# Performance work log

Hardware: AMD Instinct MI355X
Metric: run time of the kernel (lower is better)

The kernel has to match this reference:

```python
import jax, jax.numpy as jnp
import numpy as np

DIM = 1024
HEADS = 16
HEAD_DIM = DIM // HEADS
D_FF = 4 * DIM
EPS = 1e-5


def _layernorm(x, g, b):
    mu = jnp.mean(x, axis=-1, keepdims=True)
    var = jnp.mean(jnp.square(x - mu), axis=-1, keepdims=True)
    return (x - mu) * jax.lax.rsqrt(var + EPS) * g + b


def setup_inputs() -> dict:
    key = jax.random.key(0)
    ks = jax.random.split(key, 8)
    s = 0.02
    return {
        "x": jax.random.normal(ks[0], (2, 2048, DIM), dtype=jnp.float32),
        "Wqkv": jax.random.normal(ks[1], (DIM, 3 * DIM), dtype=jnp.float32) * s,
        "bqkv": jnp.zeros((3 * DIM,), dtype=jnp.float32),
        "Wout": jax.random.normal(ks[2], (DIM, DIM), dtype=jnp.float32) * s,
        "bout": jnp.zeros((DIM,), dtype=jnp.float32),
        "W1": jax.random.normal(ks[3], (DIM, D_FF), dtype=jnp.float32) * s,
        "b1": jnp.zeros((D_FF,), dtype=jnp.float32),
        "W2": jax.random.normal(ks[4], (D_FF, DIM), dtype=jnp.float32) * s,
        "b2": jnp.zeros((DIM,), dtype=jnp.float32),
        "g1": jnp.ones((DIM,), dtype=jnp.float32),
        "be1": jnp.zeros((DIM,), dtype=jnp.float32),
        "g2": jnp.ones((DIM,), dtype=jnp.float32),
        "be2": jnp.zeros((DIM,), dtype=jnp.float32),
    }


def reference(x, Wqkv, bqkv, Wout, bout, W1, b1, W2, b2, g1, be1, g2, be2):
    B, T, C = x.shape
    # --- multi-head self-attention (explicit QK^T softmax, no mask/cache) ---
    qkv = (x @ Wqkv + bqkv).reshape(B, T, 3, HEADS, HEAD_DIM)
    q = qkv[:, :, 0].transpose(0, 2, 1, 3)  # (B,H,T,hd)
    k = qkv[:, :, 1].transpose(0, 2, 1, 3)
    v = qkv[:, :, 2].transpose(0, 2, 1, 3)
    scale = HEAD_DIM ** -0.5
    scores = jnp.einsum("bhqd,bhkd->bhqk", q, k) * scale  # (B,H,T,T)
    attn = jax.nn.softmax(scores, axis=-1)
    o = jnp.einsum("bhqk,bhkd->bhqd", attn, v)
    o = o.transpose(0, 2, 1, 3).reshape(B, T, C)
    attn_out = o @ Wout + bout
    # --- Post-LN: LN applied to sublayer output, then residual ---
    x = x + _layernorm(attn_out, g1, be1)
    # --- FFN with exact GELU ---
    h = jax.nn.gelu(x @ W1 + b1, approximate=False)
    ffn_out = h @ W2 + b2
    x = x + _layernorm(ffn_out, g2, be2)
    return x
```

## Files before the change

### kernel.cpp

```cpp
#include <hip/hip_runtime.h>
#include <cstdint>
#include <cstddef>

#define DIM 1024
#define HEADS 16
#define HD 64
#define DFF 4096
#define TSEQ 2048
#define EPS 1e-5f

#define WAITCNT_VM4 0xF74
#define WAITCNT_VM0 0xF70
#define WAITCNT_VM8 0xF78
#define WAITCNT_VM4_LGKM0 0x074
#define WAITCNT_VM0_LGKM0 0x070
#define WAITCNT_LGKM0 0xC07F

typedef __bf16 bf16x8 __attribute__((ext_vector_type(8)));
typedef float floatx4 __attribute__((ext_vector_type(4)));

__device__ __forceinline__ unsigned short f2bf(float f) {
  union { float f; unsigned int u; } v; v.f = f;
  return (unsigned short)((v.u + 0x7FFFu + ((v.u >> 16) & 1u)) >> 16);
}

__device__ __forceinline__ float exp2_fast(float x) {
#if __has_builtin(__builtin_amdgcn_exp2f)
  return __builtin_amdgcn_exp2f(x);
#else
  float r;
  asm("v_exp_f32 %0, %1" : "=v"(r) : "v"(x));
  return r;
#endif
}

__device__ __forceinline__ float gelu_f(float v) {
  const float u = v * (0.7978845608f + 0.0356774081f * v * v);
  const float e = __expf(2.0f * u);
  const float t = 1.0f - 2.0f / (e + 1.0f);
  return 0.5f * v * (1.0f + t);
}

__device__ __forceinline__ void async16(const void* g, void* l) {
  __builtin_amdgcn_global_load_lds(
      (const __attribute__((address_space(1))) void*)g,
      (__attribute__((address_space(3))) void*)l, 16, 0, 0);
}

__global__ __launch_bounds__(256) void prep_all(const float* __restrict__ x,
                                                const float* __restrict__ Wqkv,
                                                const float* __restrict__ Wout,
                                                const float* __restrict__ W1,
                                                const float* __restrict__ W2,
                                                unsigned short* __restrict__ xb,
                                                unsigned short* __restrict__ WqkvT,
                                                unsigned short* __restrict__ WoutT,
                                                unsigned short* __restrict__ W1T,
                                                unsigned short* __restrict__ W2T) {
  const int bid = blockIdx.x;
  const int tid = threadIdx.x;
  if (bid < 4096) {
    const int i = bid * 256 + tid;
    float4 v = ((const float4*)x)[i];
    ushort4 o;
    o.x = f2bf(v.x); o.y = f2bf(v.y); o.z = f2bf(v.z); o.w = f2bf(v.w);
    ((ushort4*)xb)[i] = o;
    return;
  }
  int id = bid - 4096;
  const float* src; unsigned short* dst; int R, C, gx;
  if (id < 3072)      {            src = Wqkv; dst = WqkvT; R = 1024; C = 3072; gx = 96; }
  else if (id < 4096) { id -= 3072; src = Wout; dst = WoutT; R = 1024; C = 1024; gx = 32; }
  else if (id < 8192) { id -= 4096; src = W1;   dst = W1T;   R = 1024; C = 4096; gx = 128; }
  else                { id -= 8192; src = W2;   dst = W2T;   R = 4096; C = 1024; gx = 32; }
  const int c0 = (id % gx) * 32, r0 = (id / gx) * 32;
  const int tx = tid & 31, ty = tid >> 5;
  __shared__ float tile[32][33];
#pragma unroll
  for (int i = 0; i < 32; i += 8)
    tile[ty + i][tx] = src[(size_t)(r0 + ty + i) * C + c0 + tx];
  __syncthreads();
#pragma unroll
  for (int i = 0; i < 32; i += 8)
    dst[(size_t)(c0 + ty + i) * R + r0 + tx] = f2bf(tile[tx][ty + i]);
}

#define PIPELINED_KLOOP(NIT, STRIDE_EXPR)                                           \
  auto issue = [&](int s, int k0) {                                                  \
    async16(Ab0 + k0, &lds[s][tid * 8]);                                             \
    async16(Ab1 + k0, &lds[s][2048 + tid * 8]);                                      \
    async16(Bb0 + k0, &lds[s][4096 + tid * 8]);                                      \
    async16(Bb1 + k0, &lds[s][6144 + tid * 8]);                                      \
  };                                                                                 \
  issue(0, 0);                                                                       \
  issue(1, 32);                                                                      \
  int sidx = 0;                                                                      \
  for (int k = 0; k < (NIT); k++) {                                                  \
    if (k < (NIT)-1) __builtin_amdgcn_s_waitcnt(WAITCNT_VM4);                        \
    else             __builtin_amdgcn_s_waitcnt(WAITCNT_VM0);                        \
    __builtin_amdgcn_s_barrier();                                                    \
    if (k + 2 < (NIT)) {                                                             \
      int s2 = sidx + 2; if (s2 >= 3) s2 -= 3;                                       \
      issue(s2, (k + 2) * 32);                                                       \
    }                                                                                \
    bf16x8 af[4], bg[4];                                                             \
    _Pragma("unroll")                                                                \
    for (int mi = 0; mi < 4; mi++)                                                   \
      af[mi] = *(const bf16x8*)&lds[sidx][(wm + mi * 16 + l16) * 32 + quad * 8];     \
    _Pragma("unroll")                                                                \
    for (int ni = 0; ni < 4; ni++)                                                   \
      bg[ni] = *(const bf16x8*)&lds[sidx][4096 + (wn + ni * 16 + l16) * 32 + quad * 8]; \
    _Pragma("unroll")                                                                \
    for (int mi = 0; mi < 4; mi++)                                                   \
      _Pragma("unroll")                                                              \
      for (int ni = 0; ni < 4; ni++)                                                 \
        acc[mi][ni] =                                                                \
            __builtin_amdgcn_mfma_f32_16x16x32_bf16(af[mi], bg[ni], acc[mi][ni], 0, 0, 0); \
    sidx = (sidx == 2) ? 0 : sidx + 1;                                               \
  }

template <int EPI>
__global__ __launch_bounds__(256) void gemm_bt(const unsigned short* __restrict__ A,
                                               const unsigned short* __restrict__ Bt,
                                               const float* __restrict__ bias,
                                               void* __restrict__ Cout,
                                               int M, int N, int K) {
  __shared__ unsigned short lds[3][8192];
  const int tid = threadIdx.x;
  const int bm = blockIdx.y * 128, bn = blockIdx.x * 128;
  const int wave = tid >> 6, lane = tid & 63;
  const int l16 = lane & 15, quad = lane >> 4;
  const int wm = (wave >> 1) * 64, wn = (wave & 1) * 64;

  floatx4 acc[4][4] = {};

  const int srow = tid >> 2;
  const int scol = (tid & 3) * 8;

  const unsigned short* Ab0 = A + (size_t)(bm + srow) * K + scol;
  const unsigned short* Ab1 = A + (size_t)(bm + 64 + srow) * K + scol;
  const unsigned short* Bb0 = Bt + (size_t)(bn + srow) * K + scol;
  const unsigned short* Bb1 = Bt + (size_t)(bn + 64 + srow) * K + scol;

  const int nit = K >> 5;
  PIPELINED_KLOOP(nit, 32)
  __syncthreads();

  if (EPI == 0) {
#pragma unroll
    for (int ni = 0; ni < 4; ni++) {
      const int col = bn + wn + ni * 16 + l16;
      const float bv = bias[col];
#pragma unroll
      for (int mi = 0; mi < 4; mi++) {
        const int row0 = bm + wm + mi * 16 + quad * 4;
#pragma unroll
        for (int r = 0; r < 4; r++)
          ((float*)Cout)[(size_t)(row0 + r) * N + col] = acc[mi][ni][r] + bv;
      }
    }
  } else {
    unsigned short* eb = &lds[0][wave * 1152];
    float bvv[4];
#pragma unroll
    for (int ni = 0; ni < 4; ni++) bvv[ni] = bias[bn + wn + ni * 16 + l16];
    const int lrow = lane >> 2, ck = lane & 3;
#pragma unroll
    for (int mi = 0; mi < 4; mi++) {
#pragma unroll
      for (int ni = 0; ni < 4; ni++)
#pragma unroll
        for (int r = 0; r < 4; r++)
          eb[(quad * 4 + r) * 72 + ni * 16 + l16] =
              f2bf(gelu_f(acc[mi][ni][r] + bvv[ni]));
      __syncthreads();
      unsigned short* gp =
          (unsigned short*)Cout + (size_t)(bm + wm + mi * 16 + lrow) * N + bn + wn;
#pragma unroll
      for (int j = 0; j < 2; j++)
        *(uint4*)(gp + j * 32 + ck * 8) = *(const uint4*)&eb[lrow * 72 + j * 32 + ck * 8];
      __syncthreads();
    }
  }
}

__global__ __launch_bounds__(256) void gemm_splitk(const unsigned short* __restrict__ A,
                                                   const unsigned short* __restrict__ Bt,
                                                   float* __restrict__ Cp,
                                                   int M, int N, int Ktot, int Ksl) {
  __shared__ unsigned short lds[3][8192];
  const int tid = threadIdx.x;
  const int bm = blockIdx.y * 128, bn = blockIdx.x * 128;
  const int koff = blockIdx.z * Ksl;
  const int wave = tid >> 6, lane = tid & 63;
  const int l16 = lane & 15, quad = lane >> 4;
  const int wm = (wave >> 1) * 64, wn = (wave & 1) * 64;

  floatx4 acc[4][4] = {};

  const int srow = tid >> 2;
  const int scol = (tid & 3) * 8;

  const unsigned short* Ab0 = A + (size_t)(bm + srow) * Ktot + koff + scol;
  const unsigned short* Ab1 = A + (size_t)(bm + 64 + srow) * Ktot + koff + scol;
  const unsigned short* Bb0 = Bt + (size_t)(bn + srow) * Ktot + koff + scol;
  const unsigned short* Bb1 = Bt + (size_t)(bn + 64 + srow) * Ktot + koff + scol;

  const int nit = Ksl >> 5;
  PIPELINED_KLOOP(nit, 32)

  float* out = Cp + (size_t)blockIdx.z * M * (size_t)N;
#pragma unroll
  for (int ni = 0; ni < 4; ni++) {
    const int col = bn + wn + ni * 16 + l16;
#pragma unroll
    for (int mi = 0; mi < 4; mi++) {
      const int row0 = bm + wm + mi * 16 + quad * 4;
#pragma unroll
      for (int r = 0; r < 4; r++)
        out[(size_t)(row0 + r) * N + col] = acc[mi][ni][r];
    }
  }
}

__global__ __launch_bounds__(256) void gemm_qkv(const unsigned short* __restrict__ A,
                                                const unsigned short* __restrict__ Bt,
                                                const float* __restrict__ bias,
                                                unsigned short* __restrict__ Qg,
                                                unsigned short* __restrict__ Kg,
                                                unsigned short* __restrict__ Vtg) {
  const int K = 1024;
  __shared__ unsigned short lds[3][8192];
  const int tid = threadIdx.x;
  const int bm = blockIdx.y * 128, bn = blockIdx.x * 128;
  const int wave = tid >> 6, lane = tid & 63;
  const int l16 = lane & 15, quad = lane >> 4;
  const int wm = (wave >> 1) * 64, wn = (wave & 1) * 64;

  floatx4 acc[4][4] = {};

  const int srow = tid >> 2;
  const int scol = (tid & 3) * 8;

  const unsigned short* Ab0 = A + (size_t)(bm + srow) * K + scol;
  const unsigned short* Ab1 = A + (size_t)(bm + 64 + srow) * K + scol;
  const unsigned short* Bb0 = Bt + (size_t)(bn + srow) * K + scol;
  const unsigned short* Bb1 = Bt + (size_t)(bn + 64 + srow) * K + scol;

  const int nit = K >> 5;
  PIPELINED_KLOOP(nit, 32)

  const float QSCALE = 0.125f * 1.44269504089f;
#pragma unroll
  for (int ni = 0; ni < 4; ni++) {
    const int col = bn + wn + ni * 16 + l16;
    const float bv = bias[col];
    const int sec = col >> 10;
    const int cc = col & 1023;
    const int hh = cc >> 6, dd = cc & 63;
#pragma unroll
    for (int mi = 0; mi < 4; mi++) {
      const int row0 = bm + wm + mi * 16 + quad * 4;
      const int b2 = row0 >> 11, tt0 = row0 & 2047;
      if (sec == 0) {
        unsigned short* q = Qg + ((size_t)(b2 * HEADS + hh) * TSEQ + tt0) * HD + dd;
#pragma unroll
        for (int r = 0; r < 4; r++)
          q[(size_t)r * HD] = f2bf((acc[mi][ni][r] + bv) * QSCALE);
      } else if (sec == 1) {
        unsigned short* k = Kg + ((size_t)(b2 * HEADS + hh) * TSEQ + tt0) * HD + dd;
#pragma unroll
        for (int r = 0; r < 4; r++)
          k[(size_t)r * HD] = f2bf(acc[mi][ni][r] + bv);
      } else {
        ushort4 o;
        o.x = f2bf(acc[mi][ni][0] + bv);
        o.y = f2bf(acc[mi][ni][1] + bv);
        o.z = f2bf(acc[mi][ni][2] + bv);
        o.w = f2bf(acc[mi][ni][3] + bv);
        *(ushort4*)(Vtg + ((size_t)(b2 * HEADS + hh) * HD + dd) * TSEQ + tt0) = o;
      }
    }
  }
}

__global__ __launch_bounds__(256, 4) void attn_mfma(const unsigned short* __restrict__ Qg,
                                                    const unsigned short* __restrict__ Kg,
                                                    const unsigned short* __restrict__ Vtg,
                                                    unsigned short* __restrict__ ob) {
  __shared__ unsigned short QPs[64 * 64];
  __shared__ unsigned short Ks[2][64 * 64];
  __shared__ unsigned short Vs[2][64 * 64];

  const int bid = blockIdx.x;
  const int lid = (bid & 7) * 128 + (bid >> 3);
  const int qt = lid & 31;
  const int h = (lid >> 5) & 15;
  const int b = lid >> 9;
  const int tid = threadIdx.x;
  const int w = tid >> 6, lane = tid & 63, l16 = lane & 15, quad = lane >> 4;

  const int r0 = tid >> 3;
  const int c0 = (tid & 7) ^ (r0 & 7);

  const char* Qbase = (const char*)(Qg + ((size_t)(b * HEADS + h) * TSEQ + qt * 64) * HD);
  const char* Kbase = (const char*)(Kg + (size_t)(b * HEADS + h) * TSEQ * HD);
  const char* Vbase = (const char*)(Vtg + (size_t)(b * HEADS + h) * HD * TSEQ);

  auto issueKV = [&](int s, int ch) {
    const size_t koff = (size_t)ch * 64;
#pragma unroll
    for (int i = 0; i < 2; i++) {
      async16(Kbase + (koff + r0 + i * 32) * 128 + c0 * 16,
              (char*)Ks[s] + (i * 256 + tid) * 16);
      async16(Vbase + (size_t)(r0 + i * 32) * (TSEQ * 2) + koff * 2 + c0 * 16,
              (char*)Vs[s] + (i * 256 + tid) * 16);
    }
  };

#pragma unroll
  for (int i = 0; i < 2; i++)
    async16(Qbase + (size_t)(r0 + i * 32) * 128 + c0 * 16, (char*)QPs + (i * 256 + tid) * 16);
  issueKV(0, 0);
  issueKV(1, 1);

  __builtin_amdgcn_s_waitcnt(WAITCNT_VM8);
  __builtin_amdgcn_s_barrier();

  bf16x8 qf[2];
  {
    const int row = w * 16 + l16;
#pragma unroll
    for (int kt = 0; kt < 2; kt++)
      qf[kt] = *(const bf16x8*)((const char*)QPs + row * 128 +
                                (((quad + 4 * kt) ^ (row & 7)) * 16));
  }

  union { unsigned short u[8]; bf16x8 b; } onesu;
#pragma unroll
  for (int j = 0; j < 8; j++) onesu.u[j] = 0x3F80;
  const bf16x8 ones = onesu.b;

  floatx4 oacc[5] = {};
  char* PwC = (char*)QPs + w * 2048;
  const int pbase = quad * 512 + ((quad & 1) << 6) + ((l16 >> 3) << 4) + (l16 & 7) * 2;

  const int NC = TSEQ / 64;
  int sidx = 0;
  for (int ch = 0; ch < NC; ch++) {
    if (ch < NC - 1) __builtin_amdgcn_s_waitcnt(WAITCNT_VM4);
    else             __builtin_amdgcn_s_waitcnt(WAITCNT_VM0);
    __builtin_amdgcn_s_barrier();

    floatx4 sacc[4] = {};
    __builtin_amdgcn_s_setprio(1);
#pragma unroll
    for (int kt = 0; kt < 2; kt++) {
#pragma unroll
      for (int ni = 0; ni < 4; ni++) {
        const int krow = ni * 16 + l16;
        bf16x8 kf = *(const bf16x8*)((const char*)Ks[sidx] + krow * 128 +
                                     (((quad + 4 * kt) ^ (krow & 7)) * 16));
        sacc[ni] =
            __builtin_amdgcn_mfma_f32_16x16x32_bf16(qf[kt], kf, sacc[ni], 0, 0, 0);
      }
    }
    __builtin_amdgcn_s_setprio(0);

#pragma unroll
    for (int ni = 0; ni < 4; ni++)
#pragma unroll
      for (int r = 0; r < 4; r++) {
        const float p = exp2_fast(sacc[ni][r]);
        const unsigned int pu = __builtin_bit_cast(unsigned int, p);
        *((unsigned short*)(PwC +
                            (pbase ^ (r * 128 + (((ni << 1) ^ r) << 4))))) =
            (unsigned short)(pu >> 16);
      }

    __builtin_amdgcn_s_setprio(1);
#pragma unroll
    for (int kt = 0; kt < 2; kt++) {
      bf16x8 pf = *(const bf16x8*)(PwC + l16 * 128 +
                                   (((quad + 4 * kt) ^ (l16 & 7)) * 16));
#pragma unroll
      for (int nj = 0; nj < 4; nj++) {
        const int vrow = nj * 16 + l16;
        bf16x8 vf = *(const bf16x8*)((const char*)Vs[sidx] + vrow * 128 +
                                     (((quad + 4 * kt) ^ (vrow & 7)) * 16));
        oacc[nj] = __builtin_amdgcn_mfma_f32_16x16x32_bf16(pf, vf, oacc[nj], 0, 0, 0);
      }
      oacc[4] = __builtin_amdgcn_mfma_f32_16x16x32_bf16(pf, ones, oacc[4], 0, 0, 0);
    }
    __builtin_amdgcn_s_setprio(0);

    __builtin_amdgcn_s_waitcnt(WAITCNT_LGKM0);
    __builtin_amdgcn_s_barrier();
    if (ch + 2 < NC) issueKV(sidx, ch + 2);
    sidx ^= 1;
  }

#pragma unroll
  for (int r = 0; r < 4; r++) {
    const float inv = 1.0f / oacc[4][r];
    const int t = qt * 64 + w * 16 + quad * 4 + r;
    unsigned short* orow = ob + (size_t)(b * TSEQ + t) * DIM + h * HD + l16;
#pragma unroll
    for (int nj = 0; nj < 4; nj++)
      orow[nj * 16] = f2bf(oacc[nj][r] * inv);
  }
}

template <int NP, int WBF>
__global__ __launch_bounds__(256) void add_ln_red(const float* __restrict__ xin,
                                                  const float* __restrict__ parts,
                                                  const float* __restrict__ bias,
                                                  const float* __restrict__ gw,
                                                  const float* __restrict__ bw,
                                                  float* __restrict__ xout,
                                                  unsigned short* __restrict__ xbf) {
  const size_t MN = (size_t)4096 * DIM;
  const int row = blockIdx.x;
  const int tid = threadIdx.x;
  const int c = tid * 4;
  const size_t base = (size_t)row * DIM;
  float4 v = *(const float4*)(parts + base + c);
#pragma unroll
  for (int p = 1; p < NP; p++) {
    float4 t = *(const float4*)(parts + p * MN + base + c);
    v.x += t.x; v.y += t.y; v.z += t.z; v.w += t.w;
  }
  float4 bb = *(const float4*)(bias + c);
  v.x += bb.x; v.y += bb.y; v.z += bb.z; v.w += bb.w;

  float s = v.x + v.y + v.z + v.w;
  float s2 = v.x * v.x + v.y * v.y + v.z * v.z + v.w * v.w;
#pragma unroll
  for (int off = 1; off < 64; off <<= 1) {
    s += __shfl_xor(s, off);
    s2 += __shfl_xor(s2, off);
  }
  __shared__ float rsum[4], rsq[4];
  if ((tid & 63) == 0) { rsum[tid >> 6] = s; rsq[tid >> 6] = s2; }
  __syncthreads();
  s = rsum[0] + rsum[1] + rsum[2] + rsum[3];
  s2 = rsq[0] + rsq[1] + rsq[2] + rsq[3];
  const float mu = s * (1.0f / DIM);
  const float var = s2 * (1.0f / DIM) - mu * mu;
  const float rstd = rsqrtf(var + EPS);
  float4 xv = *(const float4*)(xin + base + c);
  float4 gv = *(const float4*)(gw + c);
  float4 bv = *(const float4*)(bw + c);
  float4 o;
  o.x = xv.x + (v.x - mu) * rstd * gv.x + bv.x;
  o.y = xv.y + (v.y - mu) * rstd * gv.y + bv.y;
  o.z = xv.z + (v.z - mu) * rstd * gv.z + bv.z;
  o.w = xv.w + (v.w - mu) * rstd * gv.w + bv.w;
  *(float4*)(xout + base + c) = o;
  if (WBF) {
    ushort4 ob;
    ob.x = f2bf(o.x); ob.y = f2bf(o.y); ob.z = f2bf(o.z); ob.w = f2bf(o.w);
    *(ushort4*)(xbf + base + c) = ob;
  }
}

extern "C" void kernel_launch(void* const* d_in, const int* in_sizes, int n_in,
                              void* d_out, int out_size, void* d_ws, size_t ws_size,
                              hipStream_t stream) {
  const float* x    = (const float*)d_in[0];
  const float* Wqkv = (const float*)d_in[1];
  const float* bqkv = (const float*)d_in[2];
  const float* Wout = (const float*)d_in[3];
  const float* bout = (const float*)d_in[4];
  const float* W1   = (const float*)d_in[5];
  const float* b1   = (const float*)d_in[6];
  const float* W2   = (const float*)d_in[7];
  const float* b2   = (const float*)d_in[8];
  const float* g1   = (const float*)d_in[9];
  const float* be1  = (const float*)d_in[10];
  const float* g2   = (const float*)d_in[11];
  const float* be2  = (const float*)d_in[12];

  char* w = (char*)d_ws;
  const size_t MB = 1048576;
  unsigned short* xb     = (unsigned short*)(w + 0 * MB);
  unsigned short* WqkvT  = (unsigned short*)(w + 8 * MB);
  unsigned short* WoutT  = (unsigned short*)(w + 14 * MB);
  unsigned short* W1T    = (unsigned short*)(w + 16 * MB);
  unsigned short* W2T    = (unsigned short*)(w + 24 * MB);
  unsigned short* Qb     = (unsigned short*)(w + 32 * MB);
  unsigned short* Kb     = (unsigned short*)(w + 40 * MB);
  unsigned short* Vtb    = (unsigned short*)(w + 48 * MB);
  unsigned short* obuf   = (unsigned short*)(w + 64 * MB);
  float*          atno_p = (float*)(w + 72 * MB);
  float*          x1     = (float*)(w + 104 * MB);
  unsigned short* x1b    = (unsigned short*)(w + 120 * MB);
  unsigned short* hb     = (unsigned short*)(w + 128 * MB);
  float*          ffn_p  = (float*)(w + 32 * MB);

  prep_all<<<16384, 256, 0, stream>>>(x, Wqkv, Wout, W1, W2, xb, WqkvT, WoutT, W1T, W2T);

  gemm_qkv<<<dim3(24, 32), 256, 0, stream>>>(xb, WqkvT, bqkv, Qb, Kb, Vtb);
  attn_mfma<<<1024, 256, 0, stream>>>(Qb, Kb, Vtb, obuf);
  gemm_splitk<<<dim3(8, 32, 2), 256, 0, stream>>>(obuf, WoutT, atno_p, 4096, 1024, 1024, 512);
  add_ln_red<2, 1><<<4096, 256, 0, stream>>>(x, atno_p, bout, g1, be1, x1, x1b);
  gemm_bt<1><<<dim3(32, 32), 256, 0, stream>>>(x1b, W1T, b1, hb, 4096, 4096, 1024);
  gemm_splitk<<<dim3(8, 32, 2), 256, 0, stream>>>(hb, W2T, ffn_p, 4096, 1024, 4096, 2048);
  add_ln_red<2, 0><<<4096, 256, 0, stream>>>(x1, ffn_p, b2, g2, be2, (float*)d_out, nullptr);
}
```

Measured before the change: 349.8 us.

## Split attention key chunk across wave pairs with 2x2 Q/K tiling and LDS reduction

Each wave now covers 32 query rows and half of each 64-key chunk instead of 16 query rows and the whole chunk. Every K/V fragment loaded from LDS therefore feeds two MFMAs, which cuts LDS read traffic per MFMA. At the end, the two key-half partial accumulators and row sums are combined through shared memory. The cost is more accumulator registers, which may reduce occupancy under the 4-blocks launch bound, plus an extra reduction step with two block barriers.

```diff
diff --git a/kernel.cpp b/kernel.cpp
--- a/kernel.cpp
+++ b/kernel.cpp
@@ -288,9 +288,8 @@
                                                     const unsigned short* __restrict__ Kg,
                                                     const unsigned short* __restrict__ Vtg,
                                                     unsigned short* __restrict__ ob) {
-  __shared__ unsigned short QPs[64 * 64];
-  __shared__ unsigned short Ks[2][64 * 64];
-  __shared__ unsigned short Vs[2][64 * 64];
+  __shared__ __align__(16) char smem[40960];
+  unsigned short* QPs = (unsigned short*)smem;
 
   const int bid = blockIdx.x;
   const int lid = (bid & 7) * 128 + (bid >> 3);
@@ -299,6 +298,8 @@
   const int b = lid >> 9;
   const int tid = threadIdx.x;
   const int w = tid >> 6, lane = tid & 63, l16 = lane & 15, quad = lane >> 4;
+  const int qg = w >> 1;
+  const int kh = w & 1;
 
   const int r0 = tid >> 3;
   const int c0 = (tid & 7) ^ (r0 & 7);
@@ -307,14 +308,16 @@
   const char* Kbase = (const char*)(Kg + (size_t)(b * HEADS + h) * TSEQ * HD);
   const char* Vbase = (const char*)(Vtg + (size_t)(b * HEADS + h) * HD * TSEQ);
 
+  auto Ksp = [&](int s) -> char* { return smem + 8192 + s * 8192; };
+  auto Vsp = [&](int s) -> char* { return smem + 24576 + s * 8192; };
+
   auto issueKV = [&](int s, int ch) {
     const size_t koff = (size_t)ch * 64;
 #pragma unroll
     for (int i = 0; i < 2; i++) {
-      async16(Kbase + (koff + r0 + i * 32) * 128 + c0 * 16,
-              (char*)Ks[s] + (i * 256 + tid) * 16);
+      async16(Kbase + (koff + r0 + i * 32) * 128 + c0 * 16, Ksp(s) + (i * 256 + tid) * 16);
       async16(Vbase + (size_t)(r0 + i * 32) * (TSEQ * 2) + koff * 2 + c0 * 16,
-              (char*)Vs[s] + (i * 256 + tid) * 16);
+              Vsp(s) + (i * 256 + tid) * 16);
     }
   };
 
@@ -327,23 +330,25 @@
   __builtin_amdgcn_s_waitcnt(WAITCNT_VM8);
   __builtin_amdgcn_s_barrier();
 
-  bf16x8 qf[2];
-  {
-    const int row = w * 16 + l16;
-#pragma unroll
-    for (int kt = 0; kt < 2; kt++)
-      qf[kt] = *(const bf16x8*)((const char*)QPs + row * 128 +
-                                (((quad + 4 * kt) ^ (row & 7)) * 16));
-  }
+  bf16x8 qf[2][2];
+#pragma unroll
+  for (int mi = 0; mi < 2; mi++)
+#pragma unroll
+    for (int kt = 0; kt < 2; kt++) {
+      const int row = qg * 32 + mi * 16 + l16;
+      qf[mi][kt] = *(const bf16x8*)((const char*)QPs + row * 128 +
+                                    (((quad + 4 * kt) ^ (row & 7)) * 16));
+    }
+  __builtin_amdgcn_s_waitcnt(WAITCNT_LGKM0);
+  __builtin_amdgcn_sched_barrier(0);
 
   union { unsigned short u[8]; bf16x8 b; } onesu;
 #pragma unroll
   for (int j = 0; j < 8; j++) onesu.u[j] = 0x3F80;
   const bf16x8 ones = onesu.b;
 
-  floatx4 oacc[5] = {};
-  char* PwC = (char*)QPs + w * 2048;
-  const int pbase = quad * 512 + ((quad & 1) << 6) + ((l16 >> 3) << 4) + (l16 & 7) * 2;
+  floatx4 oacc[2][5] = {};
+  char* Pw = (char*)QPs + w * 2048;
 
   const int NC = TSEQ / 64;
   int sidx = 0;
@@ -352,46 +357,56 @@
     else             __builtin_amdgcn_s_waitcnt(WAITCNT_VM0);
     __builtin_amdgcn_s_barrier();
 
-    floatx4 sacc[4] = {};
+    floatx4 sacc[2][2] = {};
     __builtin_amdgcn_s_setprio(1);
 #pragma unroll
     for (int kt = 0; kt < 2; kt++) {
 #pragma unroll
-      for (int ni = 0; ni < 4; ni++) {
-        const int krow = ni * 16 + l16;
-        bf16x8 kf = *(const bf16x8*)((const char*)Ks[sidx] + krow * 128 +
+      for (int ni = 0; ni < 2; ni++) {
+        const int krow = kh * 32 + ni * 16 + l16;
+        bf16x8 kf = *(const bf16x8*)(Ksp(sidx) + krow * 128 +
                                      (((quad + 4 * kt) ^ (krow & 7)) * 16));
-        sacc[ni] =
-            __builtin_amdgcn_mfma_f32_16x16x32_bf16(qf[kt], kf, sacc[ni], 0, 0, 0);
+#pragma unroll
+        for (int mi = 0; mi < 2; mi++)
+          sacc[mi][ni] =
+              __builtin_amdgcn_mfma_f32_16x16x32_bf16(qf[mi][kt], kf, sacc[mi][ni], 0, 0, 0);
       }
     }
     __builtin_amdgcn_s_setprio(0);
 
 #pragma unroll
-    for (int ni = 0; ni < 4; ni++)
-#pragma unroll
-      for (int r = 0; r < 4; r++) {
-        const float p = exp2_fast(sacc[ni][r]);
-        const unsigned int pu = __builtin_bit_cast(unsigned int, p);
-        *((unsigned short*)(PwC +
-                            (pbase ^ (r * 128 + (((ni << 1) ^ r) << 4))))) =
-            (unsigned short)(pu >> 16);
-      }
+    for (int mi = 0; mi < 2; mi++)
+#pragma unroll
+      for (int ni = 0; ni < 2; ni++)
+#pragma unroll
+        for (int r = 0; r < 4; r++) {
+          const float p = exp2_fast(sacc[mi][ni][r]);
+          const unsigned int pu = __builtin_bit_cast(unsigned int, p);
+          const int row = mi * 16 + quad * 4 + r;
+          *((unsigned short*)(Pw + row * 64 +
+                              (((ni * 2 + (l16 >> 3)) ^ quad) * 16) + (l16 & 7) * 2)) =
+              (unsigned short)(pu >> 16);
+        }
 
     __builtin_amdgcn_s_setprio(1);
-#pragma unroll
-    for (int kt = 0; kt < 2; kt++) {
-      bf16x8 pf = *(const bf16x8*)(PwC + l16 * 128 +
-                                   (((quad + 4 * kt) ^ (l16 & 7)) * 16));
-#pragma unroll
-      for (int nj = 0; nj < 4; nj++) {
-        const int vrow = nj * 16 + l16;
-        bf16x8 vf = *(const bf16x8*)((const char*)Vs[sidx] + vrow * 128 +
-                                     (((quad + 4 * kt) ^ (vrow & 7)) * 16));
-        oacc[nj] = __builtin_amdgcn_mfma_f32_16x16x32_bf16(pf, vf, oacc[nj], 0, 0, 0);
-      }
-      oacc[4] = __builtin_amdgcn_mfma_f32_16x16x32_bf16(pf, ones, oacc[4], 0, 0, 0);
-    }
+    bf16x8 pf[2];
+#pragma unroll
+    for (int mi = 0; mi < 2; mi++) {
+      const int prow = mi * 16 + l16;
+      pf[mi] = *(const bf16x8*)(Pw + prow * 64 + ((quad ^ ((l16 >> 2) & 3)) * 16));
+    }
+#pragma unroll
+    for (int nj = 0; nj < 4; nj++) {
+      const int vrow = nj * 16 + l16;
+      bf16x8 vf = *(const bf16x8*)(Vsp(sidx) + vrow * 128 +
+                                   (((quad + 4 * kh) ^ (vrow & 7)) * 16));
+#pragma unroll
+      for (int mi = 0; mi < 2; mi++)
+        oacc[mi][nj] = __builtin_amdgcn_mfma_f32_16x16x32_bf16(pf[mi], vf, oacc[mi][nj], 0, 0, 0);
+    }
+#pragma unroll
+    for (int mi = 0; mi < 2; mi++)
+      oacc[mi][4] = __builtin_amdgcn_mfma_f32_16x16x32_bf16(pf[mi], ones, oacc[mi][4], 0, 0, 0);
     __builtin_amdgcn_s_setprio(0);
 
     __builtin_amdgcn_s_waitcnt(WAITCNT_LGKM0);
@@ -400,14 +415,34 @@
     sidx ^= 1;
   }
 
-#pragma unroll
-  for (int r = 0; r < 4; r++) {
-    const float inv = 1.0f / oacc[4][r];
-    const int t = qt * 64 + w * 16 + quad * 4 + r;
-    unsigned short* orow = ob + (size_t)(b * TSEQ + t) * DIM + h * HD + l16;
-#pragma unroll
-    for (int nj = 0; nj < 4; nj++)
-      orow[nj * 16] = f2bf(oacc[nj][r] * inv);
+  __syncthreads();
+  float* Op = (float*)smem + qg * (32 * 66);
+  if (kh == 1) {
+#pragma unroll
+    for (int mi = 0; mi < 2; mi++)
+#pragma unroll
+      for (int r = 0; r < 4; r++) {
+        const int row = mi * 16 + quad * 4 + r;
+#pragma unroll
+        for (int nj = 0; nj < 4; nj++)
+          Op[row * 66 + nj * 16 + l16] = oacc[mi][nj][r];
+        if (l16 == 0) Op[row * 66 + 64] = oacc[mi][4][r];
+      }
+  }
+  __syncthreads();
+  if (kh == 0) {
+#pragma unroll
+    for (int mi = 0; mi < 2; mi++)
+#pragma unroll
+      for (int r = 0; r < 4; r++) {
+        const int row = mi * 16 + quad * 4 + r;
+        const float inv = 1.0f / (oacc[mi][4][r] + Op[row * 66 + 64]);
+        const int t = qt * 64 + qg * 32 + row;
+        unsigned short* orow = ob + (size_t)(b * TSEQ + t) * DIM + h * HD + l16;
+#pragma unroll
+        for (int nj = 0; nj < 4; nj++)
+          orow[nj * 16] = f2bf((oacc[mi][nj][r] + Op[row * 66 + nj * 16 + l16]) * inv);
+      }
   }
 }
 
```

Measured after the change: 349.4 us. Within noise of the previous version (-0.1%).
